# Optimization experiments

Hardware: AMD Instinct MI355X
Metric: run time of the kernel (lower is better)

## Reference

```python
import jax, jax.numpy as jnp
import numpy as np

T, B, D, H, O = 1024, 128, 512, 1024, 128

def setup_inputs() -> dict:
    key = jax.random.key(0)
    ks = jax.random.split(key, 8)
    s_in = 1.0 / np.sqrt(D)
    s_h = 1.0 / np.sqrt(H)
    return {
        "x": jax.random.normal(ks[0], (T, B, D), jnp.float32),
        "W_ih1": jax.random.normal(ks[1], (4 * H, D), jnp.float32) * s_in,
        "W_hh1": jax.random.normal(ks[2], (4 * H, H), jnp.float32) * s_h,
        "b_ih1": jnp.zeros((4 * H,), jnp.float32),
        "b_hh1": jnp.zeros((4 * H,), jnp.float32),
        "W_ih2": jax.random.normal(ks[3], (4 * H, H), jnp.float32) * s_h,
        "W_hh2": jax.random.normal(ks[4], (4 * H, H), jnp.float32) * s_h,
        "b_ih2": jnp.zeros((4 * H,), jnp.float32),
        "b_hh2": jnp.zeros((4 * H,), jnp.float32),
        "W_out": jax.random.normal(ks[5], (O, H), jnp.float32) * s_h,
        "b_out": jnp.zeros((O,), jnp.float32),
    }

def _lstm_cell(x, h, c, W_ih, W_hh, b_ih, b_hh):
    # PyTorch nn.LSTMCell: gates ordered (i, f, g, o)
    z = x @ W_ih.T + b_ih + h @ W_hh.T + b_hh  # [B, 4H]
    i, f, g, o = jnp.split(z, 4, axis=-1)
    c_new = jax.nn.sigmoid(f) * c + jax.nn.sigmoid(i) * jnp.tanh(g)
    h_new = jax.nn.sigmoid(o) * jnp.tanh(c_new)
    return h_new, c_new

def reference(x, W_ih1, W_hh1, b_ih1, b_hh1, W_ih2, W_hh2, b_ih2, b_hh2, W_out, b_out):
    Bsz = x.shape[1]
    Hdim = W_hh1.shape[1]
    zeros = jnp.zeros((Bsz, Hdim), x.dtype)

    def step(carry, x_t):
        h1, c1, h2, c2 = carry
        h1, c1 = _lstm_cell(x_t, h1, c1, W_ih1, W_hh1, b_ih1, b_hh1)
        h2, c2 = _lstm_cell(h1, h2, c2, W_ih2, W_hh2, b_ih2, b_hh2)
        y = h2 @ W_out.T + b_out  # [B, O]
        return (h1, c1, h2, c2), y

    _, ys = jax.lax.scan(step, (zeros, zeros, zeros, zeros), x)
    return ys  # [T, B, O]
```

## Files before the change

kernel.cpp:

```cpp
#include <hip/hip_runtime.h>

typedef _Float16 f16;
typedef _Float16 f16x8 __attribute__((ext_vector_type(8)));
typedef float f32x4 __attribute__((ext_vector_type(4)));

#define T_STEPS 1024
#define BATCH 128
#define DIN 512
#define HID 1024
#define OUTD 128

#define OFF_WP1 0L
#define OFF_WP2 12582912L
#define OFF_WPO 29360128L
#define OFF_B1  29622272L
#define OFF_B2  29638656L
#define OFF_H1H 29655040L
#define OFF_H2H 30179328L
#define OFF_BAR 30703616L
#define OFF_ZP  30720000L

__device__ __host__ inline int col_perm(int p) {
    int q = p >> 5, r = p & 31;
    return (r >> 3) * 1024 + q * 8 + (r & 7);
}

__global__ void pack_kernel(const float* __restrict__ Wih1, const float* __restrict__ Whh1,
                            const float* __restrict__ Wih2, const float* __restrict__ Whh2,
                            const float* __restrict__ Wout,
                            const float* __restrict__ bih1, const float* __restrict__ bhh1,
                            const float* __restrict__ bih2, const float* __restrict__ bhh2,
                            f16* Wp1, f16* Wp2, f16* Wpo, float* bias1, float* bias2,
                            f16* h1h, f16* h2h, int* bar)
{
    long idx = (long)blockIdx.x * 256 + threadIdx.x;
    const long NW1 = 786432, NW2 = 1048576, NWO = 16384;
    if (idx < NW1) {
        long blk = idx >> 6; int lane = idx & 63;
        int nb = (int)(blk / 48), kb = (int)(blk % 48);
        int p = nb * 16 + (lane & 15);
        int k = kb * 32 + (lane >> 4) * 8;
        int n = col_perm(p);
        f16x8 v;
        #pragma unroll
        for (int j = 0; j < 8; j++) {
            int kk = k + j;
            float wv = (kk < 512) ? Wih1[(size_t)n * 512 + kk] : Whh1[(size_t)n * 1024 + kk - 512];
            v[j] = (f16)wv;
        }
        *(f16x8*)(Wp1 + blk * 512 + lane * 8) = v;
        return;
    }
    idx -= NW1;
    if (idx < NW2) {
        long blk = idx >> 6; int lane = idx & 63;
        int nb = (int)(blk / 64), kb = (int)(blk % 64);
        int p = nb * 16 + (lane & 15);
        int k = kb * 32 + (lane >> 4) * 8;
        int n = col_perm(p);
        f16x8 v;
        #pragma unroll
        for (int j = 0; j < 8; j++) {
            int kk = k + j;
            float wv = (kk < 1024) ? Wih2[(size_t)n * 1024 + kk] : Whh2[(size_t)n * 1024 + kk - 1024];
            v[j] = (f16)wv;
        }
        *(f16x8*)(Wp2 + blk * 512 + lane * 8) = v;
        return;
    }
    idx -= NW2;
    if (idx < NWO) {
        long blk = idx >> 6; int lane = idx & 63;
        int nb = (int)(blk / 32), kb = (int)(blk % 32);
        int n = nb * 16 + (lane & 15);
        int k = kb * 32 + (lane >> 4) * 8;
        f16x8 v;
        #pragma unroll
        for (int j = 0; j < 8; j++) v[j] = (f16)Wout[(size_t)n * 1024 + k + j];
        *(f16x8*)(Wpo + blk * 512 + lane * 8) = v;
        return;
    }
    idx -= NWO;
    if (idx < 4096) { int n = col_perm((int)idx); bias1[idx] = bih1[n] + bhh1[n]; return; }
    idx -= 4096;
    if (idx < 4096) { int n = col_perm((int)idx); bias2[idx] = bih2[n] + bhh2[n]; return; }
    idx -= 4096;
    if (idx < 65536) {
        f16x8 z = {};
        if (idx < 32768) *(f16x8*)(h1h + idx * 8) = z;
        else             *(f16x8*)(h2h + (idx - 32768) * 8) = z;
        return;
    }
    idx -= 65536;
    if (idx < 4096) bar[idx] = 0;
}

__device__ __forceinline__ void gridbar(int* bar, int p)
{
    __syncthreads();
    const int tid = threadIdx.x;
    int* gen = bar + 2048;
    if (blockIdx.x == 0) {
        if (tid == 0)
            __hip_atomic_fetch_add(bar + 0, 1, __ATOMIC_RELAXED, __HIP_MEMORY_SCOPE_AGENT);
        if (tid < 64) {
            const int tgt = 4 * (p + 1);
            while (__hip_atomic_load(bar + tid * 32, __ATOMIC_RELAXED, __HIP_MEMORY_SCOPE_AGENT) < tgt)
                __builtin_amdgcn_s_sleep(1);
            if (tid == 0) {
                __builtin_amdgcn_fence(__ATOMIC_ACQUIRE, "agent");
                __hip_atomic_store(gen, p + 1, __ATOMIC_RELAXED, __HIP_MEMORY_SCOPE_AGENT);
            }
        }
    } else {
        if (tid == 0) {
            __hip_atomic_fetch_add(bar + (blockIdx.x & 63) * 32, 1, __ATOMIC_RELAXED, __HIP_MEMORY_SCOPE_AGENT);
            while (__hip_atomic_load(gen, __ATOMIC_RELAXED, __HIP_MEMORY_SCOPE_AGENT) < p + 1)
                __builtin_amdgcn_s_sleep(1);
            __builtin_amdgcn_fence(__ATOMIC_ACQUIRE, "agent");
        }
    }
    __syncthreads();
}

__device__ __forceinline__ void ldcopy(f16* dst, const f16* src, int nelem)
{
    for (int i = threadIdx.x * 8; i < nelem; i += 512 * 8)
        *(f16x8*)(dst + i) = *(const f16x8*)(src + i);
}

__device__ __forceinline__ void loadA_f16(f16x8 buf[8], const f16* src, int strideE, int kOff)
{
    const int lane = threadIdx.x & 63, wave = threadIdx.x >> 6;
    const int r0 = wave * 16 + (lane & 15);
    const f16* p0 = src + (size_t)r0 * strideE + kOff + (lane >> 4) * 8;
    #pragma unroll
    for (int kb = 0; kb < 8; kb++)
        buf[kb] = *(const f16x8*)(p0 + kb * 32);
}

__device__ __forceinline__ void loadA_f32(f16x8 buf[8], const float* src, int strideE, int kOff)
{
    const int lane = threadIdx.x & 63, wave = threadIdx.x >> 6;
    const int r0 = wave * 16 + (lane & 15);
    const float* p0 = src + (size_t)r0 * strideE + kOff + (lane >> 4) * 8;
    #pragma unroll
    for (int kb = 0; kb < 8; kb++) {
        float4 u0 = *(const float4*)(p0 + kb * 32);
        float4 u1 = *(const float4*)(p0 + kb * 32 + 4);
        f16x8 a;
        a[0]=(f16)u0.x; a[1]=(f16)u0.y; a[2]=(f16)u0.z; a[3]=(f16)u0.w;
        a[4]=(f16)u1.x; a[5]=(f16)u1.y; a[6]=(f16)u1.z; a[7]=(f16)u1.w;
        buf[kb] = a;
    }
}

template<bool TWON>
__device__ __forceinline__ void computeChunk(const f16* B0, const f16* B1, int kqBase,
                                             f16x8 buf[8], f32x4 acc[2])
{
    const int lane = threadIdx.x & 63;
    #pragma unroll
    for (int kb = 0; kb < 8; kb++) {
        const int kq = kqBase + kb;
        f16x8 b0 = *(const f16x8*)(B0 + (size_t)kq * 512 + lane * 8);
        acc[0] = __builtin_amdgcn_mfma_f32_16x16x32_f16(buf[kb], b0, acc[0], 0, 0, 0);
        if (TWON) {
            f16x8 b1 = *(const f16x8*)(B1 + (size_t)kq * 512 + lane * 8);
            acc[1] = __builtin_amdgcn_mfma_f32_16x16x32_f16(buf[kb], b1, acc[1], 0, 0, 0);
        }
    }
}

template<bool TWON, bool F32>
__device__ __forceinline__ void gemm_region(const void* src, int strideE, int kOff0, int kqBase, int nch,
                                            const f16* B0, const f16* B1, f32x4 acc[2])
{
    f16x8 bufA[8], bufB[8];
    if (F32) loadA_f32(bufA, (const float*)src, strideE, kOff0);
    else     loadA_f16(bufA, (const f16*)src, strideE, kOff0);
    for (int c = 0; c < nch; c += 2) {
        if (F32) loadA_f32(bufB, (const float*)src, strideE, kOff0 + (c + 1) * 256);
        else     loadA_f16(bufB, (const f16*)src, strideE, kOff0 + (c + 1) * 256);
        computeChunk<TWON>(B0, B1, kqBase + c * 8, bufA, acc);
        if (c + 2 < nch) {
            if (F32) loadA_f32(bufA, (const float*)src, strideE, kOff0 + (c + 2) * 256);
            else     loadA_f16(bufA, (const f16*)src, strideE, kOff0 + (c + 2) * 256);
        }
        computeChunk<TWON>(B0, B1, kqBase + (c + 1) * 8, bufB, acc);
    }
}

template<bool TWON>
__device__ __forceinline__ void acc_to_zl(float* zl, f32x4 acc[2])
{
    const int lane = threadIdx.x & 63, wave = threadIdx.x >> 6;
    #pragma unroll
    for (int nt = 0; nt < (TWON ? 2 : 1); nt++)
        #pragma unroll
        for (int r = 0; r < 4; r++) {
            int row = wave * 16 + (lane >> 4) * 4 + r;
            int col = nt * 16 + (lane & 15);
            zl[row * 33 + col] = acc[nt][r];
        }
}

__device__ __forceinline__ float sigm(float v) { return 1.f / (1.f + __expf(-v)); }
__device__ __forceinline__ float tanh_f(float v) { return 1.f - 2.f / (__expf(2.f * v) + 1.f); }

__device__ __forceinline__ void do_ew(const float* zl, float* cst, const float* biasp, int p0,
                                      f16* hdst, int u0)
{
    const int j = threadIdx.x & 7;
    const int bb = threadIdx.x >> 3;
    #pragma unroll
    for (int i = 0; i < 2; i++) {
        const int b = bb * 2 + i;
        float zi = zl[b * 33 + j]      + biasp[p0 + j];
        float zf = zl[b * 33 + 8 + j]  + biasp[p0 + 8 + j];
        float zg = zl[b * 33 + 16 + j] + biasp[p0 + 16 + j];
        float zo = zl[b * 33 + 24 + j] + biasp[p0 + 24 + j];
        float c  = cst[b * 9 + j];
        float cn = sigm(zf) * c + sigm(zi) * tanh_f(zg);
        float h  = sigm(zo) * tanh_f(cn);
        cst[b * 9 + j] = cn;
        f16 hv = (f16)h;
        unsigned short us = __builtin_bit_cast(unsigned short, hv);
        __hip_atomic_store((unsigned short*)(hdst + (size_t)b * HID + u0 + j), us,
                           __ATOMIC_RELAXED, __HIP_MEMORY_SCOPE_AGENT);
    }
}

__global__ void __launch_bounds__(512, 1) lstm_persist(
    const float* __restrict__ x, const float* __restrict__ b_out,
    const f16* __restrict__ Wp1, const f16* __restrict__ Wp2, const f16* __restrict__ Wpo,
    const float* __restrict__ bias1, const float* __restrict__ bias2,
    f16* h1h, f16* h2h, int* bar, float* zpart, float* __restrict__ out)
{
    __shared__ f16 Wlds[65536];
    __shared__ float zl[128 * 33];
    __shared__ float cst[128 * 9];

    const int w = blockIdx.x;
    const bool isL1 = (w < 128);
    const int wl = isL1 ? w : (w - 128);

    if (isL1) {
        ldcopy(Wlds, Wp1 + (size_t)w * 49152, 49152);
        if (w < 16)
            ldcopy(Wlds + 49152, Wpo + ((size_t)(w & 7) * 32 + (w >> 3) * 16) * 512, 8192);
    } else {
        ldcopy(Wlds, Wp2 + (size_t)wl * 65536, 65536);
    }
    for (int i = threadIdx.x; i < 128 * 9; i += 512) cst[i] = 0.f;
    __syncthreads();

    const f16* B0 = Wlds;
    const f16* B1 = isL1 ? (Wlds + 48 * 512) : (Wlds + 64 * 512);
    const f16* Bo = Wlds + 49152;

    for (int p = 0; p < T_STEPS + 3; p++) {
        if (isL1) {
            if (p < T_STEPS) {
                const int t1 = p;
                const f16* h1prev = h1h + (size_t)((t1 + 1) & 1) * (BATCH * HID);
                f32x4 acc[2] = {};
                gemm_region<true, true >(x + (size_t)t1 * BATCH * DIN, DIN, 0, 0, 2, B0, B1, acc);
                gemm_region<true, false>(h1prev, HID, 0, 16, 4, B0, B1, acc);
                __syncthreads();
                acc_to_zl<true>(zl, acc);
                __syncthreads();
                do_ew(zl, cst, bias1, w * 32, h1h + (size_t)(t1 & 1) * (BATCH * HID), w * 8);
            }
            if (w < 16 && p >= 2 && p < T_STEPS + 2) {
                const int ty = p - 2;
                const f16* h2y = h2h + (size_t)(ty & 1) * (BATCH * HID);
                f32x4 acc2[2] = {};
                gemm_region<false, false>(h2y, HID, (w >> 3) * 512, 0, 2, Bo, Bo, acc2);
                __syncthreads();
                acc_to_zl<false>(zl, acc2);
                __syncthreads();
                float* zp = zpart + (((size_t)(ty & 1) * 2 + (w >> 3)) * 8 + (w & 7)) * 2048;
                int b = threadIdx.x >> 2, oh = (threadIdx.x & 3) * 4;
                #pragma unroll
                for (int q = 0; q < 4; q++)
                    __hip_atomic_store(zp + b * 16 + oh + q, zl[b * 33 + oh + q],
                                       __ATOMIC_RELAXED, __HIP_MEMORY_SCOPE_AGENT);
            }
            if (w < 8 && p >= 3) {
                const int to = p - 3;
                const float* zp0 = zpart + (((size_t)(to & 1) * 2 + 0) * 8 + w) * 2048;
                const float* zp1 = zpart + (((size_t)(to & 1) * 2 + 1) * 8 + w) * 2048;
                int b = threadIdx.x >> 2, oh = (threadIdx.x & 3) * 4;
                const float* bo = b_out + w * 16 + oh;
                float* dst = out + ((size_t)to * BATCH + b) * OUTD + w * 16 + oh;
                #pragma unroll
                for (int q = 0; q < 4; q++) {
                    float v = zp0[b * 16 + oh + q] + zp1[b * 16 + oh + q] + bo[q];
                    __hip_atomic_store(dst + q, v, __ATOMIC_RELAXED, __HIP_MEMORY_SCOPE_AGENT);
                }
            }
        } else {
            const int t2 = p - 1;
            if (t2 >= 0 && t2 < T_STEPS) {
                const f16* h1cur  = h1h + (size_t)(t2 & 1) * (BATCH * HID);
                const f16* h2prev = h2h + (size_t)((t2 + 1) & 1) * (BATCH * HID);
                f32x4 acc[2] = {};
                gemm_region<true, false>(h1cur,  HID, 0, 0,  4, B0, B1, acc);
                gemm_region<true, false>(h2prev, HID, 0, 32, 4, B0, B1, acc);
                __syncthreads();
                acc_to_zl<true>(zl, acc);
                __syncthreads();
                do_ew(zl, cst, bias2, wl * 32, h2h + (size_t)(t2 & 1) * (BATCH * HID), wl * 8);
            }
        }
        gridbar(bar, p);
    }
}

extern "C" void kernel_launch(void* const* d_in, const int* in_sizes, int n_in,
                              void* d_out, int out_size, void* d_ws, size_t ws_size,
                              hipStream_t stream)
{
    const float* x    = (const float*)d_in[0];
    const float* Wih1 = (const float*)d_in[1];
    const float* Whh1 = (const float*)d_in[2];
    const float* bih1 = (const float*)d_in[3];
    const float* bhh1 = (const float*)d_in[4];
    const float* Wih2 = (const float*)d_in[5];
    const float* Whh2 = (const float*)d_in[6];
    const float* bih2 = (const float*)d_in[7];
    const float* bhh2 = (const float*)d_in[8];
    const float* Wout = (const float*)d_in[9];
    const float* bout = (const float*)d_in[10];

    char* ws = (char*)d_ws;
    f16*   Wp1 = (f16*)(ws + OFF_WP1);
    f16*   Wp2 = (f16*)(ws + OFF_WP2);
    f16*   Wpo = (f16*)(ws + OFF_WPO);
    float* b1  = (float*)(ws + OFF_B1);
    float* b2  = (float*)(ws + OFF_B2);
    f16*   h1h = (f16*)(ws + OFF_H1H);
    f16*   h2h = (f16*)(ws + OFF_H2H);
    int*   bar = (int*)(ws + OFF_BAR);
    float* zp  = (float*)(ws + OFF_ZP);
    float* out = (float*)d_out;

    hipLaunchKernelGGL(pack_kernel, dim3(7536), dim3(256), 0, stream,
                       Wih1, Whh1, Wih2, Whh2, Wout, bih1, bhh1, bih2, bhh2,
                       Wp1, Wp2, Wpo, b1, b2, h1h, h2h, bar);

    void* args[] = { (void*)&x, (void*)&bout, (void*)&Wp1, (void*)&Wp2, (void*)&Wpo,
                     (void*)&b1, (void*)&b2, (void*)&h1h, (void*)&h2h, (void*)&bar,
                     (void*)&zp, (void*)&out };
    hipError_t e = hipLaunchCooperativeKernel((void*)lstm_persist, dim3(256), dim3(512), args, 0, stream);
    if (e != hipSuccess) {
        hipLaunchKernelGGL(lstm_persist, dim3(256), dim3(512), 0, stream,
                           x, bout, Wp1, Wp2, Wpo, b1, b2, h1h, h2h, bar, zp, out);
    }
}
```

Before: 24.87 ms.

## Keep LSTM weights in registers, split K across waves with LDS atomic reduction

Each block's weight slice now lives in VGPRs instead of LDS. Each wave owns a K-slice and loops over all batch row tiles, and the partial sums are reduced into LDS with atomicAdd. The h buffers are stored in an MFMA-fragment-friendly tiled layout so A fragments load contiguously, and the bias is folded in by initialising the LDS accumulator. This removes the per-step LDS weight reads and the strided A loads. In exchange it adds LDS atomic contention and register pressure.

```diff
diff --git a/kernel.cpp b/kernel.cpp
--- a/kernel.cpp
+++ b/kernel.cpp
@@ -19,6 +19,7 @@
 #define OFF_H2H 30179328L
 #define OFF_BAR 30703616L
 #define OFF_ZP  30720000L
+
 
 __device__ __host__ inline int col_perm(int p) {
     int q = p >> 5, r = p & 31;
@@ -123,110 +124,175 @@
     __syncthreads();
 }
 
-__device__ __forceinline__ void ldcopy(f16* dst, const f16* src, int nelem)
-{
-    for (int i = threadIdx.x * 8; i < nelem; i += 512 * 8)
-        *(f16x8*)(dst + i) = *(const f16x8*)(src + i);
-}
-
-__device__ __forceinline__ void loadA_f16(f16x8 buf[8], const f16* src, int strideE, int kOff)
-{
-    const int lane = threadIdx.x & 63, wave = threadIdx.x >> 6;
-    const int r0 = wave * 16 + (lane & 15);
-    const f16* p0 = src + (size_t)r0 * strideE + kOff + (lane >> 4) * 8;
-    #pragma unroll
-    for (int kb = 0; kb < 8; kb++)
-        buf[kb] = *(const f16x8*)(p0 + kb * 32);
-}
-
-__device__ __forceinline__ void loadA_f32(f16x8 buf[8], const float* src, int strideE, int kOff)
-{
-    const int lane = threadIdx.x & 63, wave = threadIdx.x >> 6;
-    const int r0 = wave * 16 + (lane & 15);
-    const float* p0 = src + (size_t)r0 * strideE + kOff + (lane >> 4) * 8;
-    #pragma unroll
-    for (int kb = 0; kb < 8; kb++) {
-        float4 u0 = *(const float4*)(p0 + kb * 32);
-        float4 u1 = *(const float4*)(p0 + kb * 32 + 4);
-        f16x8 a;
-        a[0]=(f16)u0.x; a[1]=(f16)u0.y; a[2]=(f16)u0.z; a[3]=(f16)u0.w;
-        a[4]=(f16)u1.x; a[5]=(f16)u1.y; a[6]=(f16)u1.z; a[7]=(f16)u1.w;
-        buf[kb] = a;
-    }
-}
-
-template<bool TWON>
-__device__ __forceinline__ void computeChunk(const f16* B0, const f16* B1, int kqBase,
-                                             f16x8 buf[8], f32x4 acc[2])
+__device__ __forceinline__ f16x8 loadFrag(const f16* base, int m, int q)
 {
     const int lane = threadIdx.x & 63;
-    #pragma unroll
-    for (int kb = 0; kb < 8; kb++) {
-        const int kq = kqBase + kb;
-        f16x8 b0 = *(const f16x8*)(B0 + (size_t)kq * 512 + lane * 8);
-        acc[0] = __builtin_amdgcn_mfma_f32_16x16x32_f16(buf[kb], b0, acc[0], 0, 0, 0);
-        if (TWON) {
-            f16x8 b1 = *(const f16x8*)(B1 + (size_t)kq * 512 + lane * 8);
-            acc[1] = __builtin_amdgcn_mfma_f32_16x16x32_f16(buf[kb], b1, acc[1], 0, 0, 0);
-        }
-    }
-}
-
-template<bool TWON, bool F32>
-__device__ __forceinline__ void gemm_region(const void* src, int strideE, int kOff0, int kqBase, int nch,
-                                            const f16* B0, const f16* B1, f32x4 acc[2])
-{
-    f16x8 bufA[8], bufB[8];
-    if (F32) loadA_f32(bufA, (const float*)src, strideE, kOff0);
-    else     loadA_f16(bufA, (const f16*)src, strideE, kOff0);
-    for (int c = 0; c < nch; c += 2) {
-        if (F32) loadA_f32(bufB, (const float*)src, strideE, kOff0 + (c + 1) * 256);
-        else     loadA_f16(bufB, (const f16*)src, strideE, kOff0 + (c + 1) * 256);
-        computeChunk<TWON>(B0, B1, kqBase + c * 8, bufA, acc);
-        if (c + 2 < nch) {
-            if (F32) loadA_f32(bufA, (const float*)src, strideE, kOff0 + (c + 2) * 256);
-            else     loadA_f16(bufA, (const f16*)src, strideE, kOff0 + (c + 2) * 256);
-        }
-        computeChunk<TWON>(B0, B1, kqBase + (c + 1) * 8, bufB, acc);
-    }
-}
-
-template<bool TWON>
-__device__ __forceinline__ void acc_to_zl(float* zl, f32x4 acc[2])
-{
-    const int lane = threadIdx.x & 63, wave = threadIdx.x >> 6;
-    #pragma unroll
-    for (int nt = 0; nt < (TWON ? 2 : 1); nt++)
-        #pragma unroll
-        for (int r = 0; r < 4; r++) {
-            int row = wave * 16 + (lane >> 4) * 4 + r;
-            int col = nt * 16 + (lane & 15);
-            zl[row * 33 + col] = acc[nt][r];
-        }
+    return *(const f16x8*)(base + ((size_t)(m * 32 + q) * 64 + lane) * 8);
+}
+__device__ __forceinline__ f16x8 loadFragX(const float* x_t, int m, int q)
+{
+    const int lane = threadIdx.x & 63;
+    const float* p = x_t + (size_t)(m * 16 + (lane & 15)) * DIN + q * 32 + (lane >> 4) * 8;
+    float4 u0 = *(const float4*)(p);
+    float4 u1 = *(const float4*)(p + 4);
+    f16x8 a;
+    a[0]=(f16)u0.x; a[1]=(f16)u0.y; a[2]=(f16)u0.z; a[3]=(f16)u0.w;
+    a[4]=(f16)u1.x; a[5]=(f16)u1.y; a[6]=(f16)u1.z; a[7]=(f16)u1.w;
+    return a;
+}
+
+__device__ __forceinline__ void dsadd_main(float* zl, int m, f32x4 acc[2])
+{
+    const int lane = threadIdx.x & 63;
+    const int r0 = m * 16 + ((lane >> 4) << 2);
+    const int c = lane & 15;
+    #pragma unroll
+    for (int nt = 0; nt < 2; nt++)
+        #pragma unroll
+        for (int r = 0; r < 4; r++)
+            atomicAdd(&zl[(r0 + r) * 36 + nt * 16 + c], acc[nt][r]);
+}
+__device__ __forceinline__ void dsadd_y(float* zly, int m, f32x4 acc)
+{
+    const int lane = threadIdx.x & 63;
+    const int r0 = m * 16 + ((lane >> 4) << 2);
+    const int c = lane & 15;
+    #pragma unroll
+    for (int r = 0; r < 4; r++)
+        atomicAdd(&zly[(r0 + r) * 20 + c], acc[r]);
+}
+
+__device__ __forceinline__ void compute_l1(const f16x8 ax[2], const f16x8 ah[4],
+                                           const f16x8 Wx[2][2], const f16x8 Wh[4][2], f32x4 acc[2])
+{
+    #pragma unroll
+    for (int s = 0; s < 2; s++) {
+        acc[0] = __builtin_amdgcn_mfma_f32_16x16x32_f16(ax[s], Wx[s][0], acc[0], 0, 0, 0);
+        acc[1] = __builtin_amdgcn_mfma_f32_16x16x32_f16(ax[s], Wx[s][1], acc[1], 0, 0, 0);
+    }
+    #pragma unroll
+    for (int i = 0; i < 4; i++) {
+        acc[0] = __builtin_amdgcn_mfma_f32_16x16x32_f16(ah[i], Wh[i][0], acc[0], 0, 0, 0);
+        acc[1] = __builtin_amdgcn_mfma_f32_16x16x32_f16(ah[i], Wh[i][1], acc[1], 0, 0, 0);
+    }
+}
+__device__ __forceinline__ void compute_l2(const f16x8 a1[4], const f16x8 a2[4],
+                                           const f16x8 W1[4][2], const f16x8 W2[4][2], f32x4 acc[2])
+{
+    #pragma unroll
+    for (int i = 0; i < 4; i++) {
+        acc[0] = __builtin_amdgcn_mfma_f32_16x16x32_f16(a1[i], W1[i][0], acc[0], 0, 0, 0);
+        acc[1] = __builtin_amdgcn_mfma_f32_16x16x32_f16(a1[i], W1[i][1], acc[1], 0, 0, 0);
+    }
+    #pragma unroll
+    for (int i = 0; i < 4; i++) {
+        acc[0] = __builtin_amdgcn_mfma_f32_16x16x32_f16(a2[i], W2[i][0], acc[0], 0, 0, 0);
+        acc[1] = __builtin_amdgcn_mfma_f32_16x16x32_f16(a2[i], W2[i][1], acc[1], 0, 0, 0);
+    }
+}
+
+__device__ __forceinline__ void gemm_l1(const float* x_t, const f16* h1prev, int wv,
+                                        const f16x8 Wx[2][2], const f16x8 Wh[4][2], float* zl)
+{
+    const int qx0 = wv * 2, qh0 = wv * 4;
+    f16x8 axA[2], ahA[4], axB[2], ahB[4];
+    #pragma unroll
+    for (int s = 0; s < 2; s++) axA[s] = loadFragX(x_t, 0, qx0 + s);
+    #pragma unroll
+    for (int i = 0; i < 4; i++) ahA[i] = loadFrag(h1prev, 0, qh0 + i);
+    #pragma unroll
+    for (int mm = 0; mm < 8; mm += 2) {
+        #pragma unroll
+        for (int s = 0; s < 2; s++) axB[s] = loadFragX(x_t, mm + 1, qx0 + s);
+        #pragma unroll
+        for (int i = 0; i < 4; i++) ahB[i] = loadFrag(h1prev, mm + 1, qh0 + i);
+        f32x4 accA[2] = {};
+        compute_l1(axA, ahA, Wx, Wh, accA);
+        dsadd_main(zl, mm, accA);
+        if (mm + 2 < 8) {
+            #pragma unroll
+            for (int s = 0; s < 2; s++) axA[s] = loadFragX(x_t, mm + 2, qx0 + s);
+            #pragma unroll
+            for (int i = 0; i < 4; i++) ahA[i] = loadFrag(h1prev, mm + 2, qh0 + i);
+        }
+        f32x4 accB[2] = {};
+        compute_l1(axB, ahB, Wx, Wh, accB);
+        dsadd_main(zl, mm + 1, accB);
+    }
+}
+
+__device__ __forceinline__ void gemm_l2(const f16* h1cur, const f16* h2prev, int wv,
+                                        const f16x8 W1[4][2], const f16x8 W2[4][2], float* zl)
+{
+    const int q0 = wv * 4;
+    f16x8 a1A[4], a2A[4], a1B[4], a2B[4];
+    #pragma unroll
+    for (int i = 0; i < 4; i++) { a1A[i] = loadFrag(h1cur, 0, q0 + i); a2A[i] = loadFrag(h2prev, 0, q0 + i); }
+    #pragma unroll
+    for (int mm = 0; mm < 8; mm += 2) {
+        #pragma unroll
+        for (int i = 0; i < 4; i++) { a1B[i] = loadFrag(h1cur, mm + 1, q0 + i); a2B[i] = loadFrag(h2prev, mm + 1, q0 + i); }
+        f32x4 accA[2] = {};
+        compute_l2(a1A, a2A, W1, W2, accA);
+        dsadd_main(zl, mm, accA);
+        if (mm + 2 < 8) {
+            #pragma unroll
+            for (int i = 0; i < 4; i++) { a1A[i] = loadFrag(h1cur, mm + 2, q0 + i); a2A[i] = loadFrag(h2prev, mm + 2, q0 + i); }
+        }
+        f32x4 accB[2] = {};
+        compute_l2(a1B, a2B, W1, W2, accB);
+        dsadd_main(zl, mm + 1, accB);
+    }
+}
+
+__device__ __forceinline__ void gemm_y(const f16* h2y, int w, int wv, const f16x8 Wy[2], float* zly)
+{
+    const int qy0 = (w >> 3) * 16 + wv * 2;
+    f16x8 aA[2], aB[2];
+    #pragma unroll
+    for (int s = 0; s < 2; s++) aA[s] = loadFrag(h2y, 0, qy0 + s);
+    #pragma unroll
+    for (int mm = 0; mm < 8; mm += 2) {
+        #pragma unroll
+        for (int s = 0; s < 2; s++) aB[s] = loadFrag(h2y, mm + 1, qy0 + s);
+        f32x4 accA = {};
+        #pragma unroll
+        for (int s = 0; s < 2; s++) accA = __builtin_amdgcn_mfma_f32_16x16x32_f16(aA[s], Wy[s], accA, 0, 0, 0);
+        dsadd_y(zly, mm, accA);
+        if (mm + 2 < 8) {
+            #pragma unroll
+            for (int s = 0; s < 2; s++) aA[s] = loadFrag(h2y, mm + 2, qy0 + s);
+        }
+        f32x4 accB = {};
+        #pragma unroll
+        for (int s = 0; s < 2; s++) accB = __builtin_amdgcn_mfma_f32_16x16x32_f16(aB[s], Wy[s], accB, 0, 0, 0);
+        dsadd_y(zly, mm + 1, accB);
+    }
 }
 
 __device__ __forceinline__ float sigm(float v) { return 1.f / (1.f + __expf(-v)); }
 __device__ __forceinline__ float tanh_f(float v) { return 1.f - 2.f / (__expf(2.f * v) + 1.f); }
 
-__device__ __forceinline__ void do_ew(const float* zl, float* cst, const float* biasp, int p0,
-                                      f16* hdst, int u0)
+__device__ __forceinline__ void do_ew(const float* zl, float* cst, f16* hdst, int wloc)
 {
     const int j = threadIdx.x & 7;
     const int bb = threadIdx.x >> 3;
+    const int qw = wloc >> 2, w3 = wloc & 3;
     #pragma unroll
     for (int i = 0; i < 2; i++) {
         const int b = bb * 2 + i;
-        float zi = zl[b * 33 + j]      + biasp[p0 + j];
-        float zf = zl[b * 33 + 8 + j]  + biasp[p0 + 8 + j];
-        float zg = zl[b * 33 + 16 + j] + biasp[p0 + 16 + j];
-        float zo = zl[b * 33 + 24 + j] + biasp[p0 + 24 + j];
+        float zi = zl[b * 36 + j];
+        float zf = zl[b * 36 + 8 + j];
+        float zg = zl[b * 36 + 16 + j];
+        float zo = zl[b * 36 + 24 + j];
         float c  = cst[b * 9 + j];
         float cn = sigm(zf) * c + sigm(zi) * tanh_f(zg);
         float h  = sigm(zo) * tanh_f(cn);
         cst[b * 9 + j] = cn;
         f16 hv = (f16)h;
         unsigned short us = __builtin_bit_cast(unsigned short, hv);
-        __hip_atomic_store((unsigned short*)(hdst + (size_t)b * HID + u0 + j), us,
+        size_t off = (size_t)(b >> 4) * 16384 + (size_t)qw * 512 + (size_t)(w3 * 16 + (b & 15)) * 8 + j;
+        __hip_atomic_store((unsigned short*)(hdst + off), us,
                            __ATOMIC_RELAXED, __HIP_MEMORY_SCOPE_AGENT);
     }
 }
@@ -237,83 +303,121 @@
     const float* __restrict__ bias1, const float* __restrict__ bias2,
     f16* h1h, f16* h2h, int* bar, float* zpart, float* __restrict__ out)
 {
-    __shared__ f16 Wlds[65536];
-    __shared__ float zl[128 * 33];
+    __shared__ float zl[128 * 36];
+    __shared__ float zly[128 * 20];
     __shared__ float cst[128 * 9];
 
     const int w = blockIdx.x;
     const bool isL1 = (w < 128);
     const int wl = isL1 ? w : (w - 128);
-
+    const int tid = threadIdx.x;
+    const int lane = tid & 63, wv = tid >> 6;
+
+    f16x8 Wx[2][2], Wh[4][2], W1r[4][2], W2r[4][2], Wy[2];
     if (isL1) {
-        ldcopy(Wlds, Wp1 + (size_t)w * 49152, 49152);
-        if (w < 16)
-            ldcopy(Wlds + 49152, Wpo + ((size_t)(w & 7) * 32 + (w >> 3) * 16) * 512, 8192);
+        const f16* B0g = Wp1 + (size_t)w * 49152;
+        const f16* B1g = B0g + 48 * 512;
+        #pragma unroll
+        for (int s = 0; s < 2; s++) {
+            Wx[s][0] = *(const f16x8*)(B0g + (size_t)(wv * 2 + s) * 512 + lane * 8);
+            Wx[s][1] = *(const f16x8*)(B1g + (size_t)(wv * 2 + s) * 512 + lane * 8);
+        }
+        #pragma unroll
+        for (int i = 0; i < 4; i++) {
+            Wh[i][0] = *(const f16x8*)(B0g + (size_t)(16 + wv * 4 + i) * 512 + lane * 8);
+            Wh[i][1] = *(const f16x8*)(B1g + (size_t)(16 + wv * 4 + i) * 512 + lane * 8);
+        }
+        if (w < 16) {
+            #pragma unroll
+            for (int s = 0; s < 2; s++)
+                Wy[s] = *(const f16x8*)(Wpo + (size_t)((w & 7) * 32 + (w >> 3) * 16 + wv * 2 + s) * 512 + lane * 8);
+        }
     } else {
-        ldcopy(Wlds, Wp2 + (size_t)wl * 65536, 65536);
-    }
-    for (int i = threadIdx.x; i < 128 * 9; i += 512) cst[i] = 0.f;
+        const f16* B0g = Wp2 + (size_t)wl * 65536;
+        const f16* B1g = B0g + 64 * 512;
+        #pragma unroll
+        for (int i = 0; i < 4; i++) {
+            W1r[i][0] = *(const f16x8*)(B0g + (size_t)(wv * 4 + i) * 512 + lane * 8);
+            W1r[i][1] = *(const f16x8*)(B1g + (size_t)(wv * 4 + i) * 512 + lane * 8);
+            W2r[i][0] = *(const f16x8*)(B0g + (size_t)(32 + wv * 4 + i) * 512 + lane * 8);
+            W2r[i][1] = *(const f16x8*)(B1g + (size_t)(32 + wv * 4 + i) * 512 + lane * 8);
+        }
+    }
+
+    const float* biasp = (isL1 ? bias1 : bias2) + (size_t)wl * 32;
+    const int initRow = tid >> 2, initC = (tid & 3) * 8;
+    float4 bA = *(const float4*)(biasp + initC);
+    float4 bB = *(const float4*)(biasp + initC + 4);
+    float4 bo4 = {};
+    {
+        int b = tid >> 2, oh = (tid & 3) * 4;
+        if (isL1 && w < 8) bo4 = *(const float4*)(b_out + w * 16 + oh);
+        (void)b;
+    }
+    for (int i = tid; i < 128 * 9; i += 512) cst[i] = 0.f;
     __syncthreads();
 
-    const f16* B0 = Wlds;
-    const f16* B1 = isL1 ? (Wlds + 48 * 512) : (Wlds + 64 * 512);
-    const f16* Bo = Wlds + 49152;
-
     for (int p = 0; p < T_STEPS + 3; p++) {
+        if (isL1 && w < 8 && p >= 3) {
+            const int to = p - 3;
+            const float* zp0 = zpart + (((size_t)(to & 1) * 2 + 0) * 8 + w) * 2048;
+            const float* zp1 = zpart + (((size_t)(to & 1) * 2 + 1) * 8 + w) * 2048;
+            int b = tid >> 2, oh = (tid & 3) * 4;
+            float* dst = out + ((size_t)to * BATCH + b) * OUTD + w * 16 + oh;
+            #pragma unroll
+            for (int q = 0; q < 4; q++) {
+                float v = zp0[b * 16 + oh + q] + zp1[b * 16 + oh + q] + ((const float*)&bo4)[q];
+                __hip_atomic_store(dst + q, v, __ATOMIC_RELAXED, __HIP_MEMORY_SCOPE_AGENT);
+            }
+        }
+
+        *(float4*)&zl[initRow * 36 + initC]     = bA;
+        *(float4*)&zl[initRow * 36 + initC + 4] = bB;
+        if (isL1 && w < 16) {
+            int r = tid >> 2, c0 = (tid & 3) * 4;
+            float4 z = {};
+            *(float4*)&zly[r * 20 + c0] = z;
+        }
+        __syncthreads();
+
         if (isL1) {
             if (p < T_STEPS) {
                 const int t1 = p;
-                const f16* h1prev = h1h + (size_t)((t1 + 1) & 1) * (BATCH * HID);
-                f32x4 acc[2] = {};
-                gemm_region<true, true >(x + (size_t)t1 * BATCH * DIN, DIN, 0, 0, 2, B0, B1, acc);
-                gemm_region<true, false>(h1prev, HID, 0, 16, 4, B0, B1, acc);
-                __syncthreads();
-                acc_to_zl<true>(zl, acc);
-                __syncthreads();
-                do_ew(zl, cst, bias1, w * 32, h1h + (size_t)(t1 & 1) * (BATCH * HID), w * 8);
+                const f16* h1prev = h1h + (size_t)((t1 + 1) & 1) * 131072;
+                gemm_l1(x + (size_t)t1 * BATCH * DIN, h1prev, wv, Wx, Wh, zl);
             }
             if (w < 16 && p >= 2 && p < T_STEPS + 2) {
                 const int ty = p - 2;
-                const f16* h2y = h2h + (size_t)(ty & 1) * (BATCH * HID);
-                f32x4 acc2[2] = {};
-                gemm_region<false, false>(h2y, HID, (w >> 3) * 512, 0, 2, Bo, Bo, acc2);
-                __syncthreads();
-                acc_to_zl<false>(zl, acc2);
-                __syncthreads();
-                float* zp = zpart + (((size_t)(ty & 1) * 2 + (w >> 3)) * 8 + (w & 7)) * 2048;
-                int b = threadIdx.x >> 2, oh = (threadIdx.x & 3) * 4;
-                #pragma unroll
-                for (int q = 0; q < 4; q++)
-                    __hip_atomic_store(zp + b * 16 + oh + q, zl[b * 33 + oh + q],
-                                       __ATOMIC_RELAXED, __HIP_MEMORY_SCOPE_AGENT);
-            }
-            if (w < 8 && p >= 3) {
-                const int to = p - 3;
-                const float* zp0 = zpart + (((size_t)(to & 1) * 2 + 0) * 8 + w) * 2048;
-                const float* zp1 = zpart + (((size_t)(to & 1) * 2 + 1) * 8 + w) * 2048;
-                int b = threadIdx.x >> 2, oh = (threadIdx.x & 3) * 4;
-                const float* bo = b_out + w * 16 + oh;
-                float* dst = out + ((size_t)to * BATCH + b) * OUTD + w * 16 + oh;
-                #pragma unroll
-                for (int q = 0; q < 4; q++) {
-                    float v = zp0[b * 16 + oh + q] + zp1[b * 16 + oh + q] + bo[q];
-                    __hip_atomic_store(dst + q, v, __ATOMIC_RELAXED, __HIP_MEMORY_SCOPE_AGENT);
-                }
+                gemm_y(h2h + (size_t)(ty & 1) * 131072, w, wv, Wy, zly);
             }
         } else {
             const int t2 = p - 1;
             if (t2 >= 0 && t2 < T_STEPS) {
-                const f16* h1cur  = h1h + (size_t)(t2 & 1) * (BATCH * HID);
-                const f16* h2prev = h2h + (size_t)((t2 + 1) & 1) * (BATCH * HID);
-                f32x4 acc[2] = {};
-                gemm_region<true, false>(h1cur,  HID, 0, 0,  4, B0, B1, acc);
-                gemm_region<true, false>(h2prev, HID, 0, 32, 4, B0, B1, acc);
-                __syncthreads();
-                acc_to_zl<true>(zl, acc);
-                __syncthreads();
-                do_ew(zl, cst, bias2, wl * 32, h2h + (size_t)(t2 & 1) * (BATCH * HID), wl * 8);
-            }
-        }
+                const f16* h1cur  = h1h + (size_t)(t2 & 1) * 131072;
+                const f16* h2prev = h2h + (size_t)((t2 + 1) & 1) * 131072;
+                gemm_l2(h1cur, h2prev, wv, W1r, W2r, zl);
+            }
+        }
+        __syncthreads();
+
+        if (isL1) {
+            if (w < 16 && p >= 2 && p < T_STEPS + 2) {
+                const int ty = p - 2;
+                float* zp = zpart + (((size_t)(ty & 1) * 2 + (w >> 3)) * 8 + (w & 7)) * 2048;
+                int b = tid >> 2, oh = (tid & 3) * 4;
+                #pragma unroll
+                for (int q = 0; q < 4; q++)
+                    __hip_atomic_store(zp + b * 16 + oh + q, zly[b * 20 + oh + q],
+                                       __ATOMIC_RELAXED, __HIP_MEMORY_SCOPE_AGENT);
+            }
+            if (p < T_STEPS)
+                do_ew(zl, cst, h1h + (size_t)(p & 1) * 131072, w);
+        } else {
+            const int t2 = p - 1;
+            if (t2 >= 0 && t2 < T_STEPS)
+                do_ew(zl, cst, h2h + (size_t)(t2 & 1) * 131072, wl);
+        }
+
         gridbar(bar, p);
     }
 }
```

Measured after the change: 72.14 ms. 2.9x slower.

## Pre-convert x to fp16 fragment layout and unify layer GEMM pipelines

Applied to the files above, without the earlier changes.

A pre-pass in the pack kernel converts the whole input sequence x to fp16, stored in the MFMA fragment order, so layer-1 blocks can load x with contiguous 16-byte loads instead of strided fp32 loads plus conversion on every step. The x and h1 GEMM regions, and likewise the two layer-2 regions, are merged into single double-buffered loops so prefetching continues across the region boundary. Output-head partial sums and b_out are now loaded at the top of each step rather than at the end. The fp16 path is used only when the workspace is large enough, and the extra pre-pass adds memory traffic outside the recurrent loop.

```diff
diff --git a/kernel.cpp b/kernel.cpp
--- a/kernel.cpp
+++ b/kernel.cpp
@@ -19,6 +19,9 @@
 #define OFF_H2H 30179328L
 #define OFF_BAR 30703616L
 #define OFF_ZP  30720000L
+#define OFF_XF  30982144L
+#define XF_BYTES 134217728L
+#define XF_T_STRIDE 65536L
 
 __device__ __host__ inline int col_perm(int p) {
     int q = p >> 5, r = p & 31;
@@ -31,7 +34,8 @@
                             const float* __restrict__ bih1, const float* __restrict__ bhh1,
                             const float* __restrict__ bih2, const float* __restrict__ bhh2,
                             f16* Wp1, f16* Wp2, f16* Wpo, float* bias1, float* bias2,
-                            f16* h1h, f16* h2h, int* bar)
+                            f16* h1h, f16* h2h, int* bar,
+                            f16* xf, const float* __restrict__ x)
 {
     long idx = (long)blockIdx.x * 256 + threadIdx.x;
     const long NW1 = 786432, NW2 = 1048576, NWO = 16384;
@@ -92,7 +96,23 @@
         return;
     }
     idx -= 65536;
-    if (idx < 4096) bar[idx] = 0;
+    if (idx < 4096) { bar[idx] = 0; return; }
+    idx -= 4096;
+    if (xf && idx < 8388608) {
+        long g = idx;
+        int t = (int)(g >> 13);
+        int g13 = (int)(g & 8191);
+        int m = g13 >> 10, q = (g13 >> 6) & 15, lane = g13 & 63;
+        int b = m * 16 + (lane & 15);
+        int k0 = q * 32 + (lane >> 4) * 8;
+        const float* src = x + ((size_t)t * BATCH + b) * DIN + k0;
+        float4 u0 = *(const float4*)(src);
+        float4 u1 = *(const float4*)(src + 4);
+        f16x8 v;
+        v[0]=(f16)u0.x; v[1]=(f16)u0.y; v[2]=(f16)u0.z; v[3]=(f16)u0.w;
+        v[4]=(f16)u1.x; v[5]=(f16)u1.y; v[6]=(f16)u1.z; v[7]=(f16)u1.w;
+        *(f16x8*)(xf + g * 8) = v;
+    }
 }
 
 __device__ __forceinline__ void gridbar(int* bar, int p)
@@ -191,6 +211,62 @@
     }
 }
 
+template<bool XF16>
+__device__ __forceinline__ void loadChunkL1(f16x8 buf[8], const float* x_t, const f16* xf_t,
+                                            const f16* h1prev, int c)
+{
+    const int lane = threadIdx.x & 63, wave = threadIdx.x >> 6;
+    if (c < 2) {
+        if (XF16) {
+            const f16* p = xf_t + ((size_t)(wave * 16 + c * 8) << 9) + lane * 8;
+            #pragma unroll
+            for (int kb = 0; kb < 8; kb++)
+                buf[kb] = *(const f16x8*)(p + ((size_t)kb << 9));
+        } else {
+            loadA_f32(buf, x_t, DIN, c * 256);
+        }
+    } else {
+        loadA_f16(buf, h1prev, HID, (c - 2) * 256);
+    }
+}
+
+template<bool XF16>
+__device__ __forceinline__ void gemm_l1(const float* x_t, const f16* xf_t, const f16* h1prev,
+                                        const f16* B0, const f16* B1, f32x4 acc[2])
+{
+    f16x8 bufA[8], bufB[8];
+    loadChunkL1<XF16>(bufA, x_t, xf_t, h1prev, 0);
+    loadChunkL1<XF16>(bufB, x_t, xf_t, h1prev, 1);
+    #pragma unroll
+    for (int c = 0; c < 6; c += 2) {
+        computeChunk<true>(B0, B1, c * 8, bufA, acc);
+        if (c + 2 < 6) loadChunkL1<XF16>(bufA, x_t, xf_t, h1prev, c + 2);
+        computeChunk<true>(B0, B1, (c + 1) * 8, bufB, acc);
+        if (c + 3 < 6) loadChunkL1<XF16>(bufB, x_t, xf_t, h1prev, c + 3);
+    }
+}
+
+__device__ __forceinline__ void loadChunkL2(f16x8 buf[8], const f16* h1cur, const f16* h2prev, int c)
+{
+    const f16* src = (c < 4) ? h1cur : h2prev;
+    loadA_f16(buf, src, HID, (c & 3) * 256);
+}
+
+__device__ __forceinline__ void gemm_l2(const f16* h1cur, const f16* h2prev,
+                                        const f16* B0, const f16* B1, f32x4 acc[2])
+{
+    f16x8 bufA[8], bufB[8];
+    loadChunkL2(bufA, h1cur, h2prev, 0);
+    loadChunkL2(bufB, h1cur, h2prev, 1);
+    #pragma unroll
+    for (int c = 0; c < 8; c += 2) {
+        computeChunk<true>(B0, B1, c * 8, bufA, acc);
+        if (c + 2 < 8) loadChunkL2(bufA, h1cur, h2prev, c + 2);
+        computeChunk<true>(B0, B1, (c + 1) * 8, bufB, acc);
+        if (c + 3 < 8) loadChunkL2(bufB, h1cur, h2prev, c + 3);
+    }
+}
+
 template<bool TWON>
 __device__ __forceinline__ void acc_to_zl(float* zl, f32x4 acc[2])
 {
@@ -231,8 +307,9 @@
     }
 }
 
+template<bool XF16>
 __global__ void __launch_bounds__(512, 1) lstm_persist(
-    const float* __restrict__ x, const float* __restrict__ b_out,
+    const float* __restrict__ x, const f16* __restrict__ xf, const float* __restrict__ b_out,
     const f16* __restrict__ Wp1, const f16* __restrict__ Wp2, const f16* __restrict__ Wpo,
     const float* __restrict__ bias1, const float* __restrict__ bias2,
     f16* h1h, f16* h2h, int* bar, float* zpart, float* __restrict__ out)
@@ -244,6 +321,7 @@
     const int w = blockIdx.x;
     const bool isL1 = (w < 128);
     const int wl = isL1 ? w : (w - 128);
+    const int tid = threadIdx.x;
 
     if (isL1) {
         ldcopy(Wlds, Wp1 + (size_t)w * 49152, 49152);
@@ -252,7 +330,11 @@
     } else {
         ldcopy(Wlds, Wp2 + (size_t)wl * 65536, 65536);
     }
-    for (int i = threadIdx.x; i < 128 * 9; i += 512) cst[i] = 0.f;
+    for (int i = tid; i < 128 * 9; i += 512) cst[i] = 0.f;
+
+    const int ob = tid >> 2, ooh = (tid & 3) * 4;
+    float4 bo4 = {};
+    if (isL1 && w < 8) bo4 = *(const float4*)(b_out + w * 16 + ooh);
     __syncthreads();
 
     const f16* B0 = Wlds;
@@ -260,13 +342,23 @@
     const f16* Bo = Wlds + 49152;
 
     for (int p = 0; p < T_STEPS + 3; p++) {
+        const bool doOut = (isL1 && w < 8 && p >= 3);
+        float4 za = {}, zb = {};
+        if (doOut) {
+            const int to = p - 3;
+            const float* zp0 = zpart + (((size_t)(to & 1) * 2 + 0) * 8 + w) * 2048;
+            const float* zp1 = zpart + (((size_t)(to & 1) * 2 + 1) * 8 + w) * 2048;
+            za = *(const float4*)(zp0 + ob * 16 + ooh);
+            zb = *(const float4*)(zp1 + ob * 16 + ooh);
+        }
+
         if (isL1) {
             if (p < T_STEPS) {
                 const int t1 = p;
                 const f16* h1prev = h1h + (size_t)((t1 + 1) & 1) * (BATCH * HID);
                 f32x4 acc[2] = {};
-                gemm_region<true, true >(x + (size_t)t1 * BATCH * DIN, DIN, 0, 0, 2, B0, B1, acc);
-                gemm_region<true, false>(h1prev, HID, 0, 16, 4, B0, B1, acc);
+                gemm_l1<XF16>(x + (size_t)t1 * BATCH * DIN, xf + (size_t)t1 * XF_T_STRIDE,
+                              h1prev, B0, B1, acc);
                 __syncthreads();
                 acc_to_zl<true>(zl, acc);
                 __syncthreads();
@@ -281,22 +373,17 @@
                 acc_to_zl<false>(zl, acc2);
                 __syncthreads();
                 float* zp = zpart + (((size_t)(ty & 1) * 2 + (w >> 3)) * 8 + (w & 7)) * 2048;
-                int b = threadIdx.x >> 2, oh = (threadIdx.x & 3) * 4;
                 #pragma unroll
                 for (int q = 0; q < 4; q++)
-                    __hip_atomic_store(zp + b * 16 + oh + q, zl[b * 33 + oh + q],
+                    __hip_atomic_store(zp + ob * 16 + ooh + q, zl[ob * 33 + ooh + q],
                                        __ATOMIC_RELAXED, __HIP_MEMORY_SCOPE_AGENT);
             }
-            if (w < 8 && p >= 3) {
+            if (doOut) {
                 const int to = p - 3;
-                const float* zp0 = zpart + (((size_t)(to & 1) * 2 + 0) * 8 + w) * 2048;
-                const float* zp1 = zpart + (((size_t)(to & 1) * 2 + 1) * 8 + w) * 2048;
-                int b = threadIdx.x >> 2, oh = (threadIdx.x & 3) * 4;
-                const float* bo = b_out + w * 16 + oh;
-                float* dst = out + ((size_t)to * BATCH + b) * OUTD + w * 16 + oh;
+                float* dst = out + ((size_t)to * BATCH + ob) * OUTD + w * 16 + ooh;
                 #pragma unroll
                 for (int q = 0; q < 4; q++) {
-                    float v = zp0[b * 16 + oh + q] + zp1[b * 16 + oh + q] + bo[q];
+                    float v = ((const float*)&za)[q] + ((const float*)&zb)[q] + ((const float*)&bo4)[q];
                     __hip_atomic_store(dst + q, v, __ATOMIC_RELAXED, __HIP_MEMORY_SCOPE_AGENT);
                 }
             }
@@ -306,8 +393,7 @@
                 const f16* h1cur  = h1h + (size_t)(t2 & 1) * (BATCH * HID);
                 const f16* h2prev = h2h + (size_t)((t2 + 1) & 1) * (BATCH * HID);
                 f32x4 acc[2] = {};
-                gemm_region<true, false>(h1cur,  HID, 0, 0,  4, B0, B1, acc);
-                gemm_region<true, false>(h2prev, HID, 0, 32, 4, B0, B1, acc);
+                gemm_l2(h1cur, h2prev, B0, B1, acc);
                 __syncthreads();
                 acc_to_zl<true>(zl, acc);
                 __syncthreads();
@@ -346,16 +432,29 @@
     float* zp  = (float*)(ws + OFF_ZP);
     float* out = (float*)d_out;
 
-    hipLaunchKernelGGL(pack_kernel, dim3(7536), dim3(256), 0, stream,
+    const bool xf16 = (ws_size >= (size_t)(OFF_XF + XF_BYTES));
+    f16* xf = xf16 ? (f16*)(ws + OFF_XF) : (f16*)(ws + OFF_WP1);
+
+    f16* xf_pack = xf16 ? xf : nullptr;
+    int packBlocks = xf16 ? 40304 : 7536;
+    hipLaunchKernelGGL(pack_kernel, dim3(packBlocks), dim3(256), 0, stream,
                        Wih1, Whh1, Wih2, Whh2, Wout, bih1, bhh1, bih2, bhh2,
-                       Wp1, Wp2, Wpo, b1, b2, h1h, h2h, bar);
-
-    void* args[] = { (void*)&x, (void*)&bout, (void*)&Wp1, (void*)&Wp2, (void*)&Wpo,
+                       Wp1, Wp2, Wpo, b1, b2, h1h, h2h, bar, xf_pack, x);
+
+    void* args[] = { (void*)&x, (void*)&xf, (void*)&bout, (void*)&Wp1, (void*)&Wp2, (void*)&Wpo,
                      (void*)&b1, (void*)&b2, (void*)&h1h, (void*)&h2h, (void*)&bar,
                      (void*)&zp, (void*)&out };
-    hipError_t e = hipLaunchCooperativeKernel((void*)lstm_persist, dim3(256), dim3(512), args, 0, stream);
-    if (e != hipSuccess) {
-        hipLaunchKernelGGL(lstm_persist, dim3(256), dim3(512), 0, stream,
-                           x, bout, Wp1, Wp2, Wpo, b1, b2, h1h, h2h, bar, zp, out);
-    }
-}
+    if (xf16) {
+        hipError_t e = hipLaunchCooperativeKernel((void*)lstm_persist<true>, dim3(256), dim3(512), args, 0, stream);
+        if (e != hipSuccess) {
+            hipLaunchKernelGGL(lstm_persist<true>, dim3(256), dim3(512), 0, stream,
+                               x, xf, bout, Wp1, Wp2, Wpo, b1, b2, h1h, h2h, bar, zp, out);
+        }
+    } else {
+        hipError_t e = hipLaunchCooperativeKernel((void*)lstm_persist<false>, dim3(256), dim3(512), args, 0, stream);
+        if (e != hipSuccess) {
+            hipLaunchKernelGGL(lstm_persist<false>, dim3(256), dim3(512), 0, stream,
+                               x, xf, bout, Wp1, Wp2, Wpo, b1, b2, h1h, h2h, bar, zp, out);
+        }
+    }
+}
```

After: 20.49 ms. 1.21x faster.
